# Optimization experiments

Measured on AMD Instinct MI355X. Metric: run time of the kernel, lower is better.

The kernel has to match this reference:

```python
import jax, jax.numpy as jnp
import numpy as np


def setup_inputs() -> dict:
    key = jax.random.key(0)
    k1, k2 = jax.random.split(key)
    x = jax.random.normal(k1, (4, 2048, 2048), dtype=jnp.float32)
    weight = jax.random.normal(k2, (8192, 2048), dtype=jnp.float32) * 0.02
    return {"x": x, "weight": weight, "bits": 8}


def reference(x, weight, bits):
    # ---- activation quantization (per-row int8-style) ----
    scale = jnp.clip(jnp.max(jnp.abs(x), axis=-1, keepdims=True), 1e-5)  # [..., 1]
    max_val = (1 << (bits - 1)) - 1  # 127 for 8 bits
    x_q = jnp.clip(jnp.round(x * (max_val / scale)), -max_val, max_val)

    # ---- ternary weight quantization (-1, 0, 1) ----
    w_scale = jnp.mean(jnp.abs(weight))
    w_q = jnp.where(weight > 0.5 * w_scale, 1.0, 0.0) + jnp.where(
        weight < -0.5 * w_scale, -1.0, 0.0
    )

    # ---- dequantized linear: (x_q @ (w_q * w_scale)^T) / x_scale ----
    out = jnp.einsum("bsi,oi->bso", x_q, w_q * w_scale) / scale

    # ---- squared ReLU ----
    return jnp.maximum(out, 0.0) ** 2
```

## Files before the change

kernel.cpp:

```cpp
#include <hip/hip_runtime.h>
#include <hip/hip_bf16.h>

typedef __attribute__((ext_vector_type(4))) int i32x4;
typedef __attribute__((ext_vector_type(16))) int i32x16;

#define M_DIM 8192
#define N_DIM 8192
#define K_DIM 2048
#define WCOUNT (N_DIM * K_DIM)


__global__ __launch_bounds__(256) void k_abs_partial(const float* __restrict__ w,
                                                     float* __restrict__ part) {
    int tid = blockIdx.x * 256 + threadIdx.x;
    const float4* w4 = (const float4*)w;
    float s = 0.0f;
    const int total4 = WCOUNT / 4;
    for (int i = tid; i < total4; i += 2048 * 256) {
        float4 v = w4[i];
        s += fabsf(v.x) + fabsf(v.y) + fabsf(v.z) + fabsf(v.w);
    }
    #pragma unroll
    for (int off = 1; off < 64; off <<= 1) s += __shfl_xor(s, off);
    __shared__ float red[4];
    if ((threadIdx.x & 63) == 0) red[threadIdx.x >> 6] = s;
    __syncthreads();
    if (threadIdx.x == 0)
        part[blockIdx.x] = (red[0] + red[1]) + (red[2] + red[3]);
}

__global__ __launch_bounds__(256) void k_abs_final(const float* __restrict__ part,
                                                   float* __restrict__ sum) {
    int t = threadIdx.x;
    float s = 0.0f;
    #pragma unroll
    for (int i = 0; i < 8; i++) s += part[t + i * 256];
    #pragma unroll
    for (int off = 1; off < 64; off <<= 1) s += __shfl_xor(s, off);
    __shared__ float red[4];
    if ((t & 63) == 0) red[t >> 6] = s;
    __syncthreads();
    if (t == 0) sum[0] = (red[0] + red[1]) + (red[2] + red[3]);
}

__global__ __launch_bounds__(256) void k_wquant(const float* __restrict__ w,
                                                const float* __restrict__ sum,
                                                signed char* __restrict__ wqf) {
    const float thr = 0.5f * (sum[0] * (1.0f / 16777216.0f));
    const int g = blockIdx.x * 256 + threadIdx.x;
    const int n = g >> 7;
    const int kc = g & 127;
    const float4* wr = (const float4*)(w + (size_t)n * K_DIM + kc * 16);
    union { signed char c[16]; uint4 v; } pk;
    #pragma unroll
    for (int q = 0; q < 4; q++) {
        float4 v = wr[q];
        pk.c[q * 4 + 0] = v.x > thr ? 1 : (v.x < -thr ? -1 : 0);
        pk.c[q * 4 + 1] = v.y > thr ? 1 : (v.y < -thr ? -1 : 0);
        pk.c[q * 4 + 2] = v.z > thr ? 1 : (v.z < -thr ? -1 : 0);
        pk.c[q * 4 + 3] = v.w > thr ? 1 : (v.w < -thr ? -1 : 0);
    }
    *(uint4*)(wqf + (size_t)(n >> 5) * 65536 + kc * 512 + (n & 31) * 16) = pk.v;
}

__global__ __launch_bounds__(256) void k_xquant(const float* __restrict__ x,
                                                signed char* __restrict__ xqf,
                                                float* __restrict__ scale) {
    const int row = blockIdx.x;
    const int t = threadIdx.x;
    const float4* xr = (const float4*)(x + (size_t)row * K_DIM);
    float4 a = xr[t * 2];
    float4 b = xr[t * 2 + 1];
    float m = fmaxf(fmaxf(fmaxf(fabsf(a.x), fabsf(a.y)), fmaxf(fabsf(a.z), fabsf(a.w))),
                    fmaxf(fmaxf(fabsf(b.x), fabsf(b.y)), fmaxf(fabsf(b.z), fabsf(b.w))));
    #pragma unroll
    for (int off = 1; off < 64; off <<= 1) m = fmaxf(m, __shfl_xor(m, off));
    __shared__ float red[4];
    if ((t & 63) == 0) red[t >> 6] = m;
    __syncthreads();
    m = fmaxf(fmaxf(red[0], red[1]), fmaxf(red[2], red[3]));
    const float sc = fmaxf(m, 1e-5f);
    if (t == 0) scale[row] = sc;
    const float r = 127.0f / sc;
    float q[8] = {a.x, a.y, a.z, a.w, b.x, b.y, b.z, b.w};
    union { signed char c[8]; uint2 v; } pk;
    #pragma unroll
    for (int j = 0; j < 8; j++) {
        float v = rintf(q[j] * r);
        v = fminf(fmaxf(v, -127.0f), 127.0f);
        pk.c[j] = (signed char)v;
    }
    *(uint2*)(xqf + (size_t)(row >> 5) * 65536 + (t >> 1) * 512
              + (row & 31) * 16 + (t & 1) * 8) = pk.v;
}

__global__ __launch_bounds__(256) void k_coef(const float* __restrict__ sum,
                                              const float* __restrict__ scale,
                                              float* __restrict__ coef) {
    const int i = blockIdx.x * 256 + threadIdx.x;
    coef[i] = (sum[0] * (1.0f / 16777216.0f)) / scale[i];
}

#define GLDS16(g, l)                                                                   \
    __builtin_amdgcn_global_load_lds((const __attribute__((address_space(1))) void*)(g), \
                                     (__attribute__((address_space(3))) void*)(l), 16, 0, 0)

#define BAR __builtin_amdgcn_s_barrier()
#define VMW(n) asm volatile("s_waitcnt vmcnt(" #n ")" ::: "memory")

__global__ __launch_bounds__(256, 3) void k_gemm(const signed char* __restrict__ xqf,
                                                 const signed char* __restrict__ wqf,
                                                 const float* __restrict__ coef,
                                                 float* __restrict__ out) {
    __shared__ signed char lds[49152];

    const int t = threadIdx.x;
    const int lane = t & 63;
    const int wid = t >> 6;
    const int wm = wid >> 1;
    const int wn = wid & 1;
    const int l31 = lane & 31;
    const int kg = lane >> 5;

    const int bid = blockIdx.x;
    const int xcd = bid & 7;
    const int idx = bid >> 3;
    const int grp = idx >> 5;
    const int w_ = idx & 31;
    const int bcol = grp * 4 + (w_ & 3);
    const int brow = xcd * 8 + ((w_ >> 2) & 7);

    const signed char* aSrc0 = xqf + (size_t)(brow * 4 + (t >> 7)) * 65536 + (t & 127) * 16;
    const signed char* aSrc1 = xqf + (size_t)(brow * 4 + 2 + (t >> 7)) * 65536 + (t & 127) * 16;
    const signed char* bSrc0 = wqf + (size_t)(bcol * 4 + (t >> 7)) * 65536 + (t & 127) * 16;
    const signed char* bSrc1 = wqf + (size_t)(bcol * 4 + 2 + (t >> 7)) * 65536 + (t & 127) * 16;
    const int dst0 = wid * 1024;
    const int dst1 = 4096 + wid * 1024;

#define STG(bufc, kt) do {                                                         \
        GLDS16(aSrc0 + (size_t)(kt) * 2048, lds + (bufc) * 16384 + dst0);          \
        GLDS16(aSrc1 + (size_t)(kt) * 2048, lds + (bufc) * 16384 + dst1);          \
        GLDS16(bSrc0 + (size_t)(kt) * 2048, lds + (bufc) * 16384 + 8192 + dst0);   \
        GLDS16(bSrc1 + (size_t)(kt) * 2048, lds + (bufc) * 16384 + 8192 + dst1);   \
    } while (0)

    const int aRd = wm * 4096 + lane * 16;
    const int bRd = 8192 + wn * 4096 + lane * 16;

    i32x16 acc00 = (i32x16){0,0,0,0,0,0,0,0,0,0,0,0,0,0,0,0};
    i32x16 acc01 = acc00, acc10 = acc00, acc11 = acc00;

#define MMK(bufc) do {                                                             \
        const int ab = (bufc) * 16384 + aRd;                                       \
        const int bb = (bufc) * 16384 + bRd;                                       \
        i32x4 a00 = *(const i32x4*)&lds[ab];                                       \
        i32x4 a10 = *(const i32x4*)&lds[ab + 2048];                                \
        i32x4 b00 = *(const i32x4*)&lds[bb];                                       \
        i32x4 b10 = *(const i32x4*)&lds[bb + 2048];                                \
        i32x4 a01 = *(const i32x4*)&lds[ab + 1024];                                \
        i32x4 a11 = *(const i32x4*)&lds[ab + 3072];                                \
        i32x4 b01 = *(const i32x4*)&lds[bb + 1024];                                \
        i32x4 b11 = *(const i32x4*)&lds[bb + 3072];                                \
        __builtin_amdgcn_s_setprio(1);                                             \
        acc00 = __builtin_amdgcn_mfma_i32_32x32x32_i8(a00, b00, acc00, 0, 0, 0);   \
        acc01 = __builtin_amdgcn_mfma_i32_32x32x32_i8(a00, b10, acc01, 0, 0, 0);   \
        acc10 = __builtin_amdgcn_mfma_i32_32x32x32_i8(a10, b00, acc10, 0, 0, 0);   \
        acc11 = __builtin_amdgcn_mfma_i32_32x32x32_i8(a10, b10, acc11, 0, 0, 0);   \
        acc00 = __builtin_amdgcn_mfma_i32_32x32x32_i8(a01, b01, acc00, 0, 0, 0);   \
        acc01 = __builtin_amdgcn_mfma_i32_32x32x32_i8(a01, b11, acc01, 0, 0, 0);   \
        acc10 = __builtin_amdgcn_mfma_i32_32x32x32_i8(a11, b01, acc10, 0, 0, 0);   \
        acc11 = __builtin_amdgcn_mfma_i32_32x32x32_i8(a11, b11, acc11, 0, 0, 0);   \
        __builtin_amdgcn_s_setprio(0); } while (0)

#define STEP(bufc, kt) do {                                                        \
        MMK(bufc);                                                                 \
        BAR;                                                                       \
        STG(bufc, (kt) + 3);                                                       \
        VMW(8);                                                                    \
        BAR; } while (0)

    STG(0, 0); STG(1, 1); STG(2, 2);
    VMW(8);
    BAR;

    #pragma unroll 1
    for (int j = 0; j < 9; j++) {
        const int kt = 3 * j;
        STEP(0, kt);
        STEP(1, kt + 1);
        STEP(2, kt + 2);
    }
    STEP(0, 27);
    STEP(1, 28);
    MMK(2); BAR; VMW(4); BAR;
    MMK(0); BAR; VMW(0); BAR;
    MMK(1);

    const int rb = brow * 128 + wm * 64 + 4 * kg;
    const int cb = bcol * 128 + wn * 64 + l31;
    #pragma unroll
    for (int mt = 0; mt < 2; mt++) {
        const i32x16 ac0 = mt ? acc10 : acc00;
        const i32x16 ac1 = mt ? acc11 : acc01;
        #pragma unroll
        for (int r = 0; r < 16; r++) {
            const int grow = rb + mt * 32 + (r & 3) + 8 * (r >> 2);
            const float c = coef[grow];
            float v0 = (float)ac0[r] * c; v0 = fmaxf(v0, 0.0f);
            float v1 = (float)ac1[r] * c; v1 = fmaxf(v1, 0.0f);
            __builtin_nontemporal_store(v0 * v0, &out[(size_t)grow * N_DIM + cb]);
            __builtin_nontemporal_store(v1 * v1, &out[(size_t)grow * N_DIM + cb + 32]);
        }
    }
#undef STG
#undef MMK
#undef STEP
}

extern "C" void kernel_launch(void* const* d_in, const int* in_sizes, int n_in,
                              void* d_out, int out_size, void* d_ws, size_t ws_size,
                              hipStream_t stream) {
    const float* x = (const float*)d_in[0];
    const float* w = (const float*)d_in[1];
    float* out = (float*)d_out;

    char* ws = (char*)d_ws;
    float* sum   = (float*)ws;
    float* part  = (float*)(ws + 256);
    float* scale = (float*)(ws + 16384);
    float* coef  = (float*)(ws + 49152);
    signed char* xqf = (signed char*)(ws + 131072);
    signed char* wqf = (signed char*)(ws + 131072 + 16777216);

    k_abs_partial<<<2048, 256, 0, stream>>>(w, part);
    k_abs_final<<<1, 256, 0, stream>>>(part, sum);
    k_wquant<<<4096, 256, 0, stream>>>(w, sum, wqf);
    k_xquant<<<M_DIM, 256, 0, stream>>>(x, xqf, scale);
    k_coef<<<32, 256, 0, stream>>>(sum, scale, coef);
    k_gemm<<<dim3(4096), 256, 0, stream>>>(xqf, wqf, coef, out);
}
```

Baseline: 196.7 us.

## Stage GEMM epilogue through LDS for vectorized stores; fold coef into xquant

The GEMM epilogue now writes the int32 accumulators as floats into LDS, then re-reads them row-contiguously so each thread issues 16-byte nontemporal stores of full output rows, instead of scattered 4-byte stores. This targets write coalescing for the 256 MB output. The epilogue is done in two halves with extra barriers and LDS round-trips. Separately, the per-row coefficient is computed inside k_xquant, which removes the k_coef launch.

Result: no change. 199.6 us (+1.5%).

```diff
diff --git a/kernel.cpp b/kernel.cpp
--- a/kernel.cpp
+++ b/kernel.cpp
@@ -3,6 +3,7 @@
 
 typedef __attribute__((ext_vector_type(4))) int i32x4;
 typedef __attribute__((ext_vector_type(16))) int i32x16;
+typedef __attribute__((ext_vector_type(4))) float f32x4;
 
 #define M_DIM 8192
 #define N_DIM 8192
@@ -64,8 +65,9 @@
 }
 
 __global__ __launch_bounds__(256) void k_xquant(const float* __restrict__ x,
+                                                const float* __restrict__ sum,
                                                 signed char* __restrict__ xqf,
-                                                float* __restrict__ scale) {
+                                                float* __restrict__ coef) {
     const int row = blockIdx.x;
     const int t = threadIdx.x;
     const float4* xr = (const float4*)(x + (size_t)row * K_DIM);
@@ -80,7 +82,7 @@
     __syncthreads();
     m = fmaxf(fmaxf(red[0], red[1]), fmaxf(red[2], red[3]));
     const float sc = fmaxf(m, 1e-5f);
-    if (t == 0) scale[row] = sc;
+    if (t == 0) coef[row] = (sum[0] * (1.0f / 16777216.0f)) / sc;
     const float r = 127.0f / sc;
     float q[8] = {a.x, a.y, a.z, a.w, b.x, b.y, b.z, b.w};
     union { signed char c[8]; uint2 v; } pk;
@@ -94,17 +96,9 @@
               + (row & 31) * 16 + (t & 1) * 8) = pk.v;
 }
 
-__global__ __launch_bounds__(256) void k_coef(const float* __restrict__ sum,
-                                              const float* __restrict__ scale,
-                                              float* __restrict__ coef) {
-    const int i = blockIdx.x * 256 + threadIdx.x;
-    coef[i] = (sum[0] * (1.0f / 16777216.0f)) / scale[i];
-}
-
 #define GLDS16(g, l)                                                                   \
     __builtin_amdgcn_global_load_lds((const __attribute__((address_space(1))) void*)(g), \
                                      (__attribute__((address_space(3))) void*)(l), 16, 0, 0)
-
 #define BAR __builtin_amdgcn_s_barrier()
 #define VMW(n) asm volatile("s_waitcnt vmcnt(" #n ")" ::: "memory")
 
@@ -195,22 +189,43 @@
     MMK(2); BAR; VMW(4); BAR;
     MMK(0); BAR; VMW(0); BAR;
     MMK(1);
-
-    const int rb = brow * 128 + wm * 64 + 4 * kg;
-    const int cb = bcol * 128 + wn * 64 + l31;
-    #pragma unroll
-    for (int mt = 0; mt < 2; mt++) {
-        const i32x16 ac0 = mt ? acc10 : acc00;
-        const i32x16 ac1 = mt ? acc11 : acc01;
+    BAR;
+
+    float* lf = (float*)lds;
+    f32x4* lf4 = (f32x4*)lds;
+    #pragma unroll
+    for (int h = 0; h < 2; h++) {
+        if (wm == h) {
+            #pragma unroll
+            for (int mt = 0; mt < 2; mt++) {
+                const i32x16 ac0 = mt ? acc10 : acc00;
+                const i32x16 ac1 = mt ? acc11 : acc01;
+                #pragma unroll
+                for (int r = 0; r < 16; r++) {
+                    const int lrow = mt * 32 + (r & 3) + 8 * (r >> 2) + 4 * kg;
+                    lf[lrow * 128 + wn * 64 + l31]      = (float)ac0[r];
+                    lf[lrow * 128 + wn * 64 + 32 + l31] = (float)ac1[r];
+                }
+            }
+        }
+        BAR;
         #pragma unroll
-        for (int r = 0; r < 16; r++) {
-            const int grow = rb + mt * 32 + (r & 3) + 8 * (r >> 2);
+        for (int it = 0; it < 8; it++) {
+            const int idx2 = it * 256 + t;
+            const int row = idx2 >> 5;
+            const int q = idx2 & 31;
+            const int grow = brow * 128 + h * 64 + row;
             const float c = coef[grow];
-            float v0 = (float)ac0[r] * c; v0 = fmaxf(v0, 0.0f);
-            float v1 = (float)ac1[r] * c; v1 = fmaxf(v1, 0.0f);
-            __builtin_nontemporal_store(v0 * v0, &out[(size_t)grow * N_DIM + cb]);
-            __builtin_nontemporal_store(v1 * v1, &out[(size_t)grow * N_DIM + cb + 32]);
+            f32x4 v = lf4[row * 32 + q];
+            #pragma unroll
+            for (int e = 0; e < 4; e++) {
+                float z = fmaxf(v[e] * c, 0.0f);
+                v[e] = z * z;
+            }
+            __builtin_nontemporal_store(v, (f32x4*)&out[(size_t)grow * N_DIM
+                                                        + bcol * 128 + q * 4]);
         }
+        BAR;
     }
 #undef STG
 #undef MMK
@@ -227,7 +242,6 @@
     char* ws = (char*)d_ws;
     float* sum   = (float*)ws;
     float* part  = (float*)(ws + 256);
-    float* scale = (float*)(ws + 16384);
     float* coef  = (float*)(ws + 49152);
     signed char* xqf = (signed char*)(ws + 131072);
     signed char* wqf = (signed char*)(ws + 131072 + 16777216);
@@ -235,7 +249,6 @@
     k_abs_partial<<<2048, 256, 0, stream>>>(w, part);
     k_abs_final<<<1, 256, 0, stream>>>(part, sum);
     k_wquant<<<4096, 256, 0, stream>>>(w, sum, wqf);
-    k_xquant<<<M_DIM, 256, 0, stream>>>(x, xqf, scale);
-    k_coef<<<32, 256, 0, stream>>>(sum, scale, coef);
+    k_xquant<<<M_DIM, 256, 0, stream>>>(x, sum, xqf, coef);
     k_gemm<<<dim3(4096), 256, 0, stream>>>(xqf, wqf, coef, out);
 }
```

## Double-buffer GEMM LDS for higher occupancy and fold coef into xquant

Applied to the files above, without the earlier changes.

The GEMM drops from a triple-buffered 48KB LDS pipeline to a double-buffered 32KB one and raises launch bounds from 3 to 4 blocks per CU, trading prefetch depth for more resident waves. The per-row coefficient computation moves into the activation quantization kernel, which removes a separate small kernel launch and its scale buffer round-trip. Shallower prefetch can expose more global-load latency per K step.

Result: no change. 194.4 us (-1.2%).

```diff
diff --git a/kernel.cpp b/kernel.cpp
--- a/kernel.cpp
+++ b/kernel.cpp
@@ -64,8 +64,9 @@
 }
 
 __global__ __launch_bounds__(256) void k_xquant(const float* __restrict__ x,
+                                                const float* __restrict__ sum,
                                                 signed char* __restrict__ xqf,
-                                                float* __restrict__ scale) {
+                                                float* __restrict__ coef) {
     const int row = blockIdx.x;
     const int t = threadIdx.x;
     const float4* xr = (const float4*)(x + (size_t)row * K_DIM);
@@ -80,7 +81,7 @@
     __syncthreads();
     m = fmaxf(fmaxf(red[0], red[1]), fmaxf(red[2], red[3]));
     const float sc = fmaxf(m, 1e-5f);
-    if (t == 0) scale[row] = sc;
+    if (t == 0) coef[row] = (sum[0] * (1.0f / 16777216.0f)) / sc;
     const float r = 127.0f / sc;
     float q[8] = {a.x, a.y, a.z, a.w, b.x, b.y, b.z, b.w};
     union { signed char c[8]; uint2 v; } pk;
@@ -94,25 +95,17 @@
               + (row & 31) * 16 + (t & 1) * 8) = pk.v;
 }
 
-__global__ __launch_bounds__(256) void k_coef(const float* __restrict__ sum,
-                                              const float* __restrict__ scale,
-                                              float* __restrict__ coef) {
-    const int i = blockIdx.x * 256 + threadIdx.x;
-    coef[i] = (sum[0] * (1.0f / 16777216.0f)) / scale[i];
-}
-
 #define GLDS16(g, l)                                                                   \
     __builtin_amdgcn_global_load_lds((const __attribute__((address_space(1))) void*)(g), \
                                      (__attribute__((address_space(3))) void*)(l), 16, 0, 0)
-
 #define BAR __builtin_amdgcn_s_barrier()
 #define VMW(n) asm volatile("s_waitcnt vmcnt(" #n ")" ::: "memory")
 
-__global__ __launch_bounds__(256, 3) void k_gemm(const signed char* __restrict__ xqf,
+__global__ __launch_bounds__(256, 4) void k_gemm(const signed char* __restrict__ xqf,
                                                  const signed char* __restrict__ wqf,
                                                  const float* __restrict__ coef,
                                                  float* __restrict__ out) {
-    __shared__ signed char lds[49152];
+    __shared__ signed char lds[32768];
 
     const int t = threadIdx.x;
     const int lane = t & 63;
@@ -172,28 +165,24 @@
         acc11 = __builtin_amdgcn_mfma_i32_32x32x32_i8(a11, b11, acc11, 0, 0, 0);   \
         __builtin_amdgcn_s_setprio(0); } while (0)
 
-#define STEP(bufc, kt) do {                                                        \
-        MMK(bufc);                                                                 \
-        BAR;                                                                       \
-        STG(bufc, (kt) + 3);                                                       \
-        VMW(8);                                                                    \
-        BAR; } while (0)
-
-    STG(0, 0); STG(1, 1); STG(2, 2);
-    VMW(8);
+    STG(0, 0);
+    STG(1, 1);
+    VMW(4);
     BAR;
 
     #pragma unroll 1
-    for (int j = 0; j < 9; j++) {
-        const int kt = 3 * j;
-        STEP(0, kt);
-        STEP(1, kt + 1);
-        STEP(2, kt + 2);
-    }
-    STEP(0, 27);
-    STEP(1, 28);
-    MMK(2); BAR; VMW(4); BAR;
-    MMK(0); BAR; VMW(0); BAR;
+    for (int j = 0; j < 15; j++) {
+        const int kt = 2 * j;
+        MMK(0); BAR;
+        STG(0, kt + 2); VMW(4);
+        BAR;
+        MMK(1); BAR;
+        STG(1, kt + 3); VMW(4);
+        BAR;
+    }
+    MMK(0); BAR;
+    VMW(0);
+    BAR;
     MMK(1);
 
     const int rb = brow * 128 + wm * 64 + 4 * kg;
@@ -214,7 +203,6 @@
     }
 #undef STG
 #undef MMK
-#undef STEP
 }
 
 extern "C" void kernel_launch(void* const* d_in, const int* in_sizes, int n_in,
@@ -227,7 +215,6 @@
     char* ws = (char*)d_ws;
     float* sum   = (float*)ws;
     float* part  = (float*)(ws + 256);
-    float* scale = (float*)(ws + 16384);
     float* coef  = (float*)(ws + 49152);
     signed char* xqf = (signed char*)(ws + 131072);
     signed char* wqf = (signed char*)(ws + 131072 + 16777216);
@@ -235,7 +222,6 @@
     k_abs_partial<<<2048, 256, 0, stream>>>(w, part);
     k_abs_final<<<1, 256, 0, stream>>>(part, sum);
     k_wquant<<<4096, 256, 0, stream>>>(w, sum, wqf);
-    k_xquant<<<M_DIM, 256, 0, stream>>>(x, xqf, scale);
-    k_coef<<<32, 256, 0, stream>>>(sum, scale, coef);
+    k_xquant<<<M_DIM, 256, 0, stream>>>(x, sum, xqf, coef);
     k_gemm<<<dim3(4096), 256, 0, stream>>>(xqf, wqf, coef, out);
 }
```

## Enlarge GEMM tile to 256x128 and fold coef computation into xquant

Applied to the files above, without the earlier changes.

The int8 MFMA GEMM block tile grows from 128x128 to 256x128, so each wave now holds eight 32x32 accumulators instead of four. LDS per block rises to 72KB with a triple-buffered pipeline, occupancy drops to 2 blocks per CU, and the grid halves. The aim is more reuse of each staged B tile and fewer global loads per MFMA. Separately, the k_coef kernel is removed and its per-row coefficient is computed inside k_xquant, saving one launch. The cost is extra register pressure and lower occupancy, which may hurt latency hiding.

Result: no change. 194.9 us (-0.9%).

```diff
diff --git a/kernel.cpp b/kernel.cpp
--- a/kernel.cpp
+++ b/kernel.cpp
@@ -64,8 +64,9 @@
 }
 
 __global__ __launch_bounds__(256) void k_xquant(const float* __restrict__ x,
+                                                const float* __restrict__ sum,
                                                 signed char* __restrict__ xqf,
-                                                float* __restrict__ scale) {
+                                                float* __restrict__ coef) {
     const int row = blockIdx.x;
     const int t = threadIdx.x;
     const float4* xr = (const float4*)(x + (size_t)row * K_DIM);
@@ -80,7 +81,7 @@
     __syncthreads();
     m = fmaxf(fmaxf(red[0], red[1]), fmaxf(red[2], red[3]));
     const float sc = fmaxf(m, 1e-5f);
-    if (t == 0) scale[row] = sc;
+    if (t == 0) coef[row] = (sum[0] * (1.0f / 16777216.0f)) / sc;
     const float r = 127.0f / sc;
     float q[8] = {a.x, a.y, a.z, a.w, b.x, b.y, b.z, b.w};
     union { signed char c[8]; uint2 v; } pk;
@@ -94,25 +95,17 @@
               + (row & 31) * 16 + (t & 1) * 8) = pk.v;
 }
 
-__global__ __launch_bounds__(256) void k_coef(const float* __restrict__ sum,
-                                              const float* __restrict__ scale,
-                                              float* __restrict__ coef) {
-    const int i = blockIdx.x * 256 + threadIdx.x;
-    coef[i] = (sum[0] * (1.0f / 16777216.0f)) / scale[i];
-}
-
 #define GLDS16(g, l)                                                                   \
     __builtin_amdgcn_global_load_lds((const __attribute__((address_space(1))) void*)(g), \
                                      (__attribute__((address_space(3))) void*)(l), 16, 0, 0)
-
 #define BAR __builtin_amdgcn_s_barrier()
 #define VMW(n) asm volatile("s_waitcnt vmcnt(" #n ")" ::: "memory")
 
-__global__ __launch_bounds__(256, 3) void k_gemm(const signed char* __restrict__ xqf,
+__global__ __launch_bounds__(256, 2) void k_gemm(const signed char* __restrict__ xqf,
                                                  const signed char* __restrict__ wqf,
                                                  const float* __restrict__ coef,
                                                  float* __restrict__ out) {
-    __shared__ signed char lds[49152];
+    __shared__ signed char lds[73728];
 
     const int t = threadIdx.x;
     const int lane = t & 63;
@@ -125,62 +118,70 @@
     const int bid = blockIdx.x;
     const int xcd = bid & 7;
     const int idx = bid >> 3;
-    const int grp = idx >> 5;
-    const int w_ = idx & 31;
+    const int grp = idx >> 4;
+    const int w_ = idx & 15;
     const int bcol = grp * 4 + (w_ & 3);
-    const int brow = xcd * 8 + ((w_ >> 2) & 7);
-
-    const signed char* aSrc0 = xqf + (size_t)(brow * 4 + (t >> 7)) * 65536 + (t & 127) * 16;
-    const signed char* aSrc1 = xqf + (size_t)(brow * 4 + 2 + (t >> 7)) * 65536 + (t & 127) * 16;
-    const signed char* bSrc0 = wqf + (size_t)(bcol * 4 + (t >> 7)) * 65536 + (t & 127) * 16;
-    const signed char* bSrc1 = wqf + (size_t)(bcol * 4 + 2 + (t >> 7)) * 65536 + (t & 127) * 16;
-    const int dst0 = wid * 1024;
-    const int dst1 = 4096 + wid * 1024;
+    const int brow = xcd * 4 + (w_ >> 2);
+
+    const int tsel = t >> 7;
+    const size_t aT0 = (size_t)(brow * 8 + 0 + tsel) * 65536 + (t & 127) * 16;
+    const size_t aT1 = (size_t)(brow * 8 + 2 + tsel) * 65536 + (t & 127) * 16;
+    const size_t aT2 = (size_t)(brow * 8 + 4 + tsel) * 65536 + (t & 127) * 16;
+    const size_t aT3 = (size_t)(brow * 8 + 6 + tsel) * 65536 + (t & 127) * 16;
+    const size_t bT0 = (size_t)(bcol * 4 + 0 + tsel) * 65536 + (t & 127) * 16;
+    const size_t bT1 = (size_t)(bcol * 4 + 2 + tsel) * 65536 + (t & 127) * 16;
+    const int dA = wid * 1024;
+    const int dB = 16384 + wid * 1024;
 
 #define STG(bufc, kt) do {                                                         \
-        GLDS16(aSrc0 + (size_t)(kt) * 2048, lds + (bufc) * 16384 + dst0);          \
-        GLDS16(aSrc1 + (size_t)(kt) * 2048, lds + (bufc) * 16384 + dst1);          \
-        GLDS16(bSrc0 + (size_t)(kt) * 2048, lds + (bufc) * 16384 + 8192 + dst0);   \
-        GLDS16(bSrc1 + (size_t)(kt) * 2048, lds + (bufc) * 16384 + 8192 + dst1);   \
+        const size_t ko_ = (size_t)(kt) * 2048;                                    \
+        GLDS16(xqf + aT0 + ko_, lds + (bufc) * 24576 + dA);                        \
+        GLDS16(xqf + aT1 + ko_, lds + (bufc) * 24576 + dA + 4096);                 \
+        GLDS16(xqf + aT2 + ko_, lds + (bufc) * 24576 + dA + 8192);                 \
+        GLDS16(xqf + aT3 + ko_, lds + (bufc) * 24576 + dA + 12288);                \
+        GLDS16(wqf + bT0 + ko_, lds + (bufc) * 24576 + dB);                        \
+        GLDS16(wqf + bT1 + ko_, lds + (bufc) * 24576 + dB + 4096);                 \
     } while (0)
 
-    const int aRd = wm * 4096 + lane * 16;
-    const int bRd = 8192 + wn * 4096 + lane * 16;
-
-    i32x16 acc00 = (i32x16){0,0,0,0,0,0,0,0,0,0,0,0,0,0,0,0};
-    i32x16 acc01 = acc00, acc10 = acc00, acc11 = acc00;
+    const int aRd = wm * 8192 + lane * 16;
+    const int bRd = 16384 + wn * 4096 + lane * 16;
+
+    i32x16 c00 = (i32x16){0,0,0,0,0,0,0,0,0,0,0,0,0,0,0,0};
+    i32x16 c01 = c00, c10 = c00, c11 = c00;
+    i32x16 c20 = c00, c21 = c00, c30 = c00, c31 = c00;
 
 #define MMK(bufc) do {                                                             \
-        const int ab = (bufc) * 16384 + aRd;                                       \
-        const int bb = (bufc) * 16384 + bRd;                                       \
-        i32x4 a00 = *(const i32x4*)&lds[ab];                                       \
-        i32x4 a10 = *(const i32x4*)&lds[ab + 2048];                                \
-        i32x4 b00 = *(const i32x4*)&lds[bb];                                       \
-        i32x4 b10 = *(const i32x4*)&lds[bb + 2048];                                \
-        i32x4 a01 = *(const i32x4*)&lds[ab + 1024];                                \
-        i32x4 a11 = *(const i32x4*)&lds[ab + 3072];                                \
-        i32x4 b01 = *(const i32x4*)&lds[bb + 1024];                                \
-        i32x4 b11 = *(const i32x4*)&lds[bb + 3072];                                \
-        __builtin_amdgcn_s_setprio(1);                                             \
-        acc00 = __builtin_amdgcn_mfma_i32_32x32x32_i8(a00, b00, acc00, 0, 0, 0);   \
-        acc01 = __builtin_amdgcn_mfma_i32_32x32x32_i8(a00, b10, acc01, 0, 0, 0);   \
-        acc10 = __builtin_amdgcn_mfma_i32_32x32x32_i8(a10, b00, acc10, 0, 0, 0);   \
-        acc11 = __builtin_amdgcn_mfma_i32_32x32x32_i8(a10, b10, acc11, 0, 0, 0);   \
-        acc00 = __builtin_amdgcn_mfma_i32_32x32x32_i8(a01, b01, acc00, 0, 0, 0);   \
-        acc01 = __builtin_amdgcn_mfma_i32_32x32x32_i8(a01, b11, acc01, 0, 0, 0);   \
-        acc10 = __builtin_amdgcn_mfma_i32_32x32x32_i8(a11, b01, acc10, 0, 0, 0);   \
-        acc11 = __builtin_amdgcn_mfma_i32_32x32x32_i8(a11, b11, acc11, 0, 0, 0);   \
-        __builtin_amdgcn_s_setprio(0); } while (0)
+        const int ab = (bufc) * 24576 + aRd;                                       \
+        const int bb = (bufc) * 24576 + bRd;                                       \
+        _Pragma("unroll")                                                          \
+        for (int ks = 0; ks < 2; ks++) {                                           \
+            i32x4 a0 = *(const i32x4*)&lds[ab + ks * 1024];                        \
+            i32x4 a1 = *(const i32x4*)&lds[ab + 2048 + ks * 1024];                 \
+            i32x4 a2 = *(const i32x4*)&lds[ab + 4096 + ks * 1024];                 \
+            i32x4 a3 = *(const i32x4*)&lds[ab + 6144 + ks * 1024];                 \
+            i32x4 b0 = *(const i32x4*)&lds[bb + ks * 1024];                        \
+            i32x4 b1 = *(const i32x4*)&lds[bb + 2048 + ks * 1024];                 \
+            __builtin_amdgcn_s_setprio(1);                                         \
+            c00 = __builtin_amdgcn_mfma_i32_32x32x32_i8(a0, b0, c00, 0, 0, 0);     \
+            c01 = __builtin_amdgcn_mfma_i32_32x32x32_i8(a0, b1, c01, 0, 0, 0);     \
+            c10 = __builtin_amdgcn_mfma_i32_32x32x32_i8(a1, b0, c10, 0, 0, 0);     \
+            c11 = __builtin_amdgcn_mfma_i32_32x32x32_i8(a1, b1, c11, 0, 0, 0);     \
+            c20 = __builtin_amdgcn_mfma_i32_32x32x32_i8(a2, b0, c20, 0, 0, 0);     \
+            c21 = __builtin_amdgcn_mfma_i32_32x32x32_i8(a2, b1, c21, 0, 0, 0);     \
+            c30 = __builtin_amdgcn_mfma_i32_32x32x32_i8(a3, b0, c30, 0, 0, 0);     \
+            c31 = __builtin_amdgcn_mfma_i32_32x32x32_i8(a3, b1, c31, 0, 0, 0);     \
+            __builtin_amdgcn_s_setprio(0);                                         \
+        } } while (0)
 
 #define STEP(bufc, kt) do {                                                        \
         MMK(bufc);                                                                 \
         BAR;                                                                       \
         STG(bufc, (kt) + 3);                                                       \
-        VMW(8);                                                                    \
+        VMW(12);                                                                   \
         BAR; } while (0)
 
     STG(0, 0); STG(1, 1); STG(2, 2);
-    VMW(8);
+    VMW(12);
     BAR;
 
     #pragma unroll 1
@@ -192,16 +193,16 @@
     }
     STEP(0, 27);
     STEP(1, 28);
-    MMK(2); BAR; VMW(4); BAR;
+    MMK(2); BAR; VMW(6); BAR;
     MMK(0); BAR; VMW(0); BAR;
     MMK(1);
 
-    const int rb = brow * 128 + wm * 64 + 4 * kg;
+    const int rb = brow * 256 + wm * 128 + 4 * kg;
     const int cb = bcol * 128 + wn * 64 + l31;
     #pragma unroll
-    for (int mt = 0; mt < 2; mt++) {
-        const i32x16 ac0 = mt ? acc10 : acc00;
-        const i32x16 ac1 = mt ? acc11 : acc01;
+    for (int mt = 0; mt < 4; mt++) {
+        const i32x16 ac0 = (mt == 0) ? c00 : (mt == 1) ? c10 : (mt == 2) ? c20 : c30;
+        const i32x16 ac1 = (mt == 0) ? c01 : (mt == 1) ? c11 : (mt == 2) ? c21 : c31;
         #pragma unroll
         for (int r = 0; r < 16; r++) {
             const int grow = rb + mt * 32 + (r & 3) + 8 * (r >> 2);
@@ -227,7 +228,6 @@
     char* ws = (char*)d_ws;
     float* sum   = (float*)ws;
     float* part  = (float*)(ws + 256);
-    float* scale = (float*)(ws + 16384);
     float* coef  = (float*)(ws + 49152);
     signed char* xqf = (signed char*)(ws + 131072);
     signed char* wqf = (signed char*)(ws + 131072 + 16777216);
@@ -235,7 +235,6 @@
     k_abs_partial<<<2048, 256, 0, stream>>>(w, part);
     k_abs_final<<<1, 256, 0, stream>>>(part, sum);
     k_wquant<<<4096, 256, 0, stream>>>(w, sum, wqf);
-    k_xquant<<<M_DIM, 256, 0, stream>>>(x, xqf, scale);
-    k_coef<<<32, 256, 0, stream>>>(sum, scale, coef);
-    k_gemm<<<dim3(4096), 256, 0, stream>>>(xqf, wqf, coef, out);
-}
+    k_xquant<<<M_DIM, 256, 0, stream>>>(x, sum, xqf, coef);
+    k_gemm<<<dim3(2048), 256, 0, stream>>>(xqf, wqf, coef, out);
+}
```
